# Performance work log

Measured on AMD Instinct MI355X. Metric: run time of the kernel, lower is better.

## Reference

```python
import jax, jax.numpy as jnp
import numpy as np
from jax import lax

N, IC, OC, K, SDIM, H, W = 16, 512, 512, 3, 512, 32, 32
PAD, STRIDE, LR = 1, 1, 1.0
WEIGHT_SCALER = 1.0 / np.sqrt(IC * K * K) * LR   # equalized-lr conv scale
FC_SCALER = 1.0 / np.sqrt(SDIM) * LR             # equalized-lr fc scale


def setup_inputs() -> dict:
    key = jax.random.key(0)
    k1, k2, k3 = jax.random.split(key, 3)
    x = jax.random.normal(k1, (N, IC, H, W), dtype=jnp.float32)
    style = jax.random.normal(k2, (N, SDIM), dtype=jnp.float32)
    weight = jax.random.normal(k3, (OC, IC, K, K), dtype=jnp.float32)  # std = 1/lr = 1
    fc_weight = jax.random.normal(jax.random.fold_in(key, 10), (IC, SDIM), dtype=jnp.float32)
    fc_bias = jnp.zeros((IC,), dtype=jnp.float32)
    return {"x": x, "style": style, "weight": weight,
            "fc_weight": fc_weight, "fc_bias": fc_bias}


def reference(x, style, weight, fc_weight, fc_bias):
    # EqualizedFullyConnect + AddChannelwiseBias, then +1 -> modulation rates [N, iC]
    mod = jnp.einsum('ns,cs->nc', style, fc_weight) * FC_SCALER + fc_bias * LR + 1.0
    # modulated per-sample weight [N, oC, iC, kH, kW]
    w = WEIGHT_SCALER * weight[None] * mod[:, None, :, None, None]
    # demodulate: rsqrt of sum of squares over (iC, kH, kW)
    demod = lax.rsqrt(jnp.sum(w * w, axis=(2, 3, 4)) + 1e-8)  # [N, oC]
    w = w * demod[:, :, None, None, None]
    # grouped conv with groups=N == per-sample conv: vmap over batch
    def conv1(xi, wi):
        # xi: [iC,H,W], wi: [oC,iC,kH,kW]
        return lax.conv_general_dilated(
            xi[None], wi, window_strides=(STRIDE, STRIDE),
            padding=((PAD, PAD), (PAD, PAD)),
            dimension_numbers=('NCHW', 'OIHW', 'NCHW'))[0]
    out = jax.vmap(conv1)(x, w)  # [N, oC, H, W]
    return out
```

## Files before the change

### kernel.cpp

```cpp
#include <hip/hip_runtime.h>
#include <hip/hip_bf16.h>

#define N_    16
#define IC_   512
#define OC_   512
#define SDIM_ 512
#define H_    32
#define W_    32
#define HW_   1024

#define FC_SCALER 0.04419417382415922f
#define WS_       0.014731391274719738f
#define WS2_      (1.0f/4608.0f)

typedef __attribute__((__ext_vector_type__(8)))  __bf16 bf16x8;
typedef __attribute__((__ext_vector_type__(16))) float  f32x16;
typedef __attribute__((__ext_vector_type__(4)))  int    i32x4;

typedef __attribute__((address_space(1))) const unsigned int GInt;
typedef __attribute__((address_space(3))) unsigned int LInt;

#define WAIT4()  asm volatile("s_waitcnt vmcnt(4)"  ::: "memory")
#define WAIT14() asm volatile("s_waitcnt vmcnt(14)" ::: "memory")
#define WAIT0()  asm volatile("s_waitcnt vmcnt(0)"  ::: "memory")

__device__ __forceinline__ unsigned short f2bf(float f) {
    unsigned int u = __builtin_bit_cast(unsigned int, f);
    unsigned int r = (u + 0x7FFFu + ((u >> 16) & 1u)) >> 16;
    return (unsigned short)r;
}

__global__ void k_mod(const float* __restrict__ style, const float* __restrict__ fcw,
                      const float* __restrict__ fcb, float* __restrict__ mod) {
    int gid = blockIdx.x * blockDim.x + threadIdx.x;
    int wid = gid >> 6, lane = gid & 63;
    if (wid >= N_ * IC_) return;
    int n = wid >> 9, c = wid & 511;
    const float4* sp = (const float4*)(style + n * SDIM_);
    const float4* wp = (const float4*)(fcw + (size_t)c * SDIM_);
    float acc = 0.f;
    for (int i = lane; i < SDIM_ / 4; i += 64) {
        float4 a = sp[i], b = wp[i];
        acc += a.x*b.x + a.y*b.y + a.z*b.z + a.w*b.w;
    }
#pragma unroll
    for (int off = 32; off; off >>= 1) acc += __shfl_xor(acc, off);
    if (lane == 0) mod[wid] = acc * FC_SCALER + fcb[c] + 1.0f;
}

__global__ void k_wprep(const float* __restrict__ w, unsigned short* __restrict__ wt,
                        float* __restrict__ wsq) {
    int tid = blockIdx.x * blockDim.x + threadIdx.x;
    int oc = tid >> 9, ic = tid & 511;
    int og = oc >> 7, ocl = oc & 127;
    int icc = ic >> 6, k6 = ic & 63, ks = k6 >> 3, i8 = k6 & 7;
    float s = 0.f;
#pragma unroll
    for (int t = 0; t < 9; t++) {
        float v = w[(size_t)tid * 9 + t];
        s += v * v;
        size_t off = ((((size_t)t * 4 + og) * 8 + icc) * 8192)
                   + (size_t)ks * 1024 + ocl * 8 + i8;
        wt[off] = f2bf(v);
    }
    wsq[tid] = s;
}

__global__ void k_demod(const float* __restrict__ mod, const float* __restrict__ wsq,
                        float* __restrict__ demod_ws) {
    int gid = blockIdx.x * blockDim.x + threadIdx.x;
    int wid = gid >> 6, lane = gid & 63;
    if (wid >= N_ * OC_) return;
    int n = wid >> 9, oc = wid & 511;
    const float4* mp = (const float4*)(mod + n * IC_);
    const float4* qp = (const float4*)(wsq + (size_t)oc * IC_);
    float acc = 0.f;
    for (int i = lane; i < IC_ / 4; i += 64) {
        float4 m = mp[i], q = qp[i];
        acc += m.x*m.x*q.x + m.y*m.y*q.y + m.z*m.z*q.z + m.w*m.w*q.w;
    }
#pragma unroll
    for (int off = 32; off; off >>= 1) acc += __shfl_xor(acc, off);
    if (lane == 0) {
        float s = WS2_ * acc + 1e-8f;
        demod_ws[wid] = WS_ / sqrtf(s);
    }
}

__global__ void k_premod(const float* __restrict__ x, const float* __restrict__ mod,
                         unsigned short* __restrict__ xm) {
    __shared__ __align__(16) unsigned short t_lds[64][80];
    int bx = blockIdx.x;
    int n = bx >> 7, hwt = (bx >> 3) & 15, ict = bx & 7;
    int hw0 = hwt * 64, ic0 = ict * 64;
    int tid = threadIdx.x, lane = tid & 63, ty = tid >> 6;
#pragma unroll
    for (int jj = 0; jj < 16; jj++) {
        int icl = ty * 16 + jj;
        float v = x[(size_t)(n * IC_ + ic0 + icl) * HW_ + hw0 + lane]
                  * mod[n * IC_ + ic0 + icl];
        t_lds[lane][icl] = f2bf(v);
    }
    __syncthreads();
    int xcol = tid & 31, ks = tid >> 5;
#pragma unroll
    for (int rep = 0; rep < 2; rep++) {
        int hwl = rep * 32 + xcol;
        i32x4 v = *(const i32x4*)&t_lds[hwl][ks * 8];
        int y = (hw0 >> 5) + rep;
        size_t off = ((((size_t)n * 8 + ict) * 32 + y) * 8 + ks) * 256 + xcol * 8;
        *(i32x4*)(xm + off) = v;
    }
}

__global__ __launch_bounds__(256, 1)
void k_conv(const unsigned short* __restrict__ xm, const unsigned short* __restrict__ wt,
            const float* __restrict__ demod_ws, float* __restrict__ out) {
    __shared__ __align__(16) unsigned short xt[2][10 * 2048];
    __shared__ __align__(16) unsigned short wb[3][8192];
    __shared__ __align__(16) unsigned short trash[512];
    __shared__ __align__(16) float zslot[4];
    __shared__ float s_demod[128];

    int bx = blockIdx.x;
    int octg = bx >> 6, n = (bx >> 2) & 15, spt = bx & 3;
    int oc0 = octg * 128, y0 = spt * 8;
    int tid = threadIdx.x, lane = tid & 63, wid = tid >> 6;
    int l31 = lane & 31, lhi = lane >> 5;
    int wr = wid >> 1, wc = wid & 1;

    if (tid < 128) s_demod[tid] = demod_ws[n * OC_ + oc0 + tid];
    __builtin_amdgcn_sched_barrier(0);

    if (tid == 0) { i32x4 z = {}; *(i32x4*)zslot = z; }
    if (spt == 0) {
        i32x4 z = {};
        *(i32x4*)&xt[0][tid * 8] = z;
        *(i32x4*)&xt[1][tid * 8] = z;
    }
    if (spt == 3) {
        i32x4 z = {};
        *(i32x4*)&xt[0][9 * 2048 + tid * 8] = z;
        *(i32x4*)&xt[1][9 * 2048 + tid * 8] = z;
    }

    const unsigned short* xsrc_n = xm + (size_t)n * (8 * 32 * 2048);

    auto stage_x = [&](int buf, int icc) {
        for (int wl = wid; wl < 40; wl += 4) {
            int rr = wl >> 2, q = wl & 3;
            int y = y0 - 1 + rr;
            int yc = y < 0 ? 0 : (y > 31 ? 31 : y);
            bool oob = (unsigned)y >= 32u;
            const unsigned short* g =
                xsrc_n + ((size_t)icc * 32 + yc) * 2048 + q * 512 + lane * 8;
            unsigned short* l = oob ? (unsigned short*)trash
                                    : &xt[buf][rr * 2048 + q * 512];
            __builtin_amdgcn_global_load_lds((GInt*)g, (LInt*)l, 16, 0, 0);
        }
    };
    auto stage_w = [&](int slot, int tap, int icc) {
        const unsigned short* wsrcc = wt + (((size_t)tap * 4 + octg) * 8 + icc) * 8192;
#pragma unroll
        for (int k = 0; k < 4; k++) {
            int wl = wid + k * 4;
            const unsigned short* g = wsrcc + wl * 512 + lane * 8;
            unsigned short* l = &wb[slot][wl * 512];
            __builtin_amdgcn_global_load_lds((GInt*)g, (LInt*)l, 16, 0, 0);
        }
    };

    f32x16 acc[2][4] = {};

    stage_x(0, 0);
    stage_w(0, 0, 0);
    stage_w(1, 1, 0);
    asm volatile("s_waitcnt lgkmcnt(0)" ::: "memory");

    int xb = 0;
#pragma unroll 1
    for (int icc = 0; icc < 8; icc++) {
#pragma unroll
        for (int t = 0; t < 9; t++) {
            if (t == 1 || t == 2) { if (icc < 7) WAIT14(); else WAIT4(); }
            else if (icc == 7 && t == 8) WAIT0();
            else WAIT4();
            __builtin_amdgcn_s_barrier();
            {
                int tt = t + 2;
                int wicc = icc + (tt >= 9);
                int wtap = tt >= 9 ? tt - 9 : tt;
                if (wicc < 8) stage_w((t + 2) % 3, wtap, wicc);
            }
            if (t == 0 && icc < 7) stage_x(xb ^ 1, icc + 1);

            const int dy = t / 3, dx = t % 3;
            const unsigned short* wbp = wb[t % 3];
            const unsigned short* xtp = xt[xb];
            int colbase = l31 + dx - 1;
            bool oobc = (unsigned)colbase >= 32u;
#pragma unroll
            for (int kk = 0; kk < 4; kk++) {
                int ks = kk * 2 + lhi;
                bf16x8 af[2], bfr[4];
#pragma unroll
                for (int fo = 0; fo < 2; fo++)
                    af[fo] = *(const bf16x8*)(wbp + ks * 1024 + (wr * 64 + fo * 32 + l31) * 8);
#pragma unroll
                for (int fs = 0; fs < 4; fs++) {
                    int rr = wc * 4 + fs + dy;
                    const unsigned short* p = oobc
                        ? (const unsigned short*)zslot
                        : (xtp + rr * 2048 + ks * 256 + colbase * 8);
                    bfr[fs] = *(const bf16x8*)p;
                }
                __builtin_amdgcn_s_setprio(1);
#pragma unroll
                for (int fo = 0; fo < 2; fo++)
#pragma unroll
                    for (int fs = 0; fs < 4; fs++)
                        acc[fo][fs] = __builtin_amdgcn_mfma_f32_32x32x16_bf16(
                            af[fo], bfr[fs], acc[fo][fs], 0, 0, 0);
                __builtin_amdgcn_s_setprio(0);
            }
        }
        xb ^= 1;
    }

#pragma unroll
    for (int fo = 0; fo < 2; fo++) {
#pragma unroll
        for (int fs = 0; fs < 4; fs++) {
            int y = y0 + wc * 4 + fs;
#pragma unroll
            for (int r = 0; r < 16; r++) {
                int row = (r & 3) + 8 * (r >> 2) + 4 * lhi;
                int ocl = wr * 64 + fo * 32 + row;
                float v = acc[fo][fs][r] * s_demod[ocl];
                out[((size_t)(n * OC_ + oc0 + ocl) * H_ + y) * W_ + l31] = v;
            }
        }
    }
}

extern "C" void kernel_launch(void* const* d_in, const int* in_sizes, int n_in,
                              void* d_out, int out_size, void* d_ws, size_t ws_size,
                              hipStream_t stream) {
    const float* x      = (const float*)d_in[0];
    const float* style  = (const float*)d_in[1];
    const float* weight = (const float*)d_in[2];
    const float* fcw    = (const float*)d_in[3];
    const float* fcb    = (const float*)d_in[4];
    float* out = (float*)d_out;

    char* ws = (char*)d_ws;
    float*          mod   = (float*)ws;
    float*          demod = (float*)(ws + 32768);
    float*          wsq   = (float*)(ws + 65536);
    unsigned short* wtb   = (unsigned short*)(ws + 65536 + 1048576);
    unsigned short* xmb   = (unsigned short*)(ws + 65536 + 1048576 + 4718592);

    k_mod   <<<2048, 256, 0, stream>>>(style, fcw, fcb, mod);
    k_wprep <<<1024, 256, 0, stream>>>(weight, wtb, wsq);
    k_demod <<<2048, 256, 0, stream>>>(mod, wsq, demod);
    k_premod<<<2048, 256, 0, stream>>>(x, mod, xmb);
    k_conv  <<<256,  256, 0, stream>>>(xmb, wtb, demod, out);
}
```

Before: 105.7 us.

## Split K across two wave groups and restage conv per tap column

The conv kernel goes from 256 to 512 threads. The two halves of the block each take half of every 64-channel K slice (intra-block split-K), and their partial accumulators are reduced through LDS at the end. The weight and activation layouts are re-tiled into 32-channel chunks. Each stage now loads three taps of one column and reuses six activation rows across dy, with a simpler double-buffered wait scheme. Block indices are also remapped so neighbouring blocks share n and spatial tile. The aim is more waves to hide latency and fewer LDS reads per MFMA, at the cost of a reduction epilogue and more barriers.

```diff
diff --git a/kernel.cpp b/kernel.cpp
--- a/kernel.cpp
+++ b/kernel.cpp
@@ -20,9 +20,8 @@
 typedef __attribute__((address_space(1))) const unsigned int GInt;
 typedef __attribute__((address_space(3))) unsigned int LInt;
 
-#define WAIT4()  asm volatile("s_waitcnt vmcnt(4)"  ::: "memory")
-#define WAIT14() asm volatile("s_waitcnt vmcnt(14)" ::: "memory")
 #define WAIT0()  asm volatile("s_waitcnt vmcnt(0)"  ::: "memory")
+#define WAIT3()  asm volatile("s_waitcnt vmcnt(3)"  ::: "memory")
 
 __device__ __forceinline__ unsigned short f2bf(float f) {
     unsigned int u = __builtin_bit_cast(unsigned int, f);
@@ -53,14 +52,14 @@
     int tid = blockIdx.x * blockDim.x + threadIdx.x;
     int oc = tid >> 9, ic = tid & 511;
     int og = oc >> 7, ocl = oc & 127;
-    int icc = ic >> 6, k6 = ic & 63, ks = k6 >> 3, i8 = k6 & 7;
+    int icc = ic >> 5, ks = (ic >> 3) & 3, i8 = ic & 7;
     float s = 0.f;
 #pragma unroll
     for (int t = 0; t < 9; t++) {
         float v = w[(size_t)tid * 9 + t];
         s += v * v;
-        size_t off = ((((size_t)t * 4 + og) * 8 + icc) * 8192)
-                   + (size_t)ks * 1024 + ocl * 8 + i8;
+        size_t off = ((((size_t)t * 4 + og) * 16 + icc) * 4 + ks) * 1024
+                   + (size_t)ocl * 8 + i8;
         wt[off] = f2bf(v);
     }
     wsq[tid] = s;
@@ -102,70 +101,79 @@
         t_lds[lane][icl] = f2bf(v);
     }
     __syncthreads();
-    int xcol = tid & 31, ks = tid >> 5;
+    int xcol = tid & 31, ks64 = tid >> 5;
+    int icc = ict * 2 + (ks64 >> 2), ks = ks64 & 3;
 #pragma unroll
     for (int rep = 0; rep < 2; rep++) {
         int hwl = rep * 32 + xcol;
-        i32x4 v = *(const i32x4*)&t_lds[hwl][ks * 8];
+        i32x4 v = *(const i32x4*)&t_lds[hwl][ks64 * 8];
         int y = (hw0 >> 5) + rep;
-        size_t off = ((((size_t)n * 8 + ict) * 32 + y) * 8 + ks) * 256 + xcol * 8;
+        size_t off = ((((size_t)n * 16 + icc) * 32 + y) * 4 + ks) * 256 + xcol * 8;
         *(i32x4*)(xm + off) = v;
     }
 }
 
-__global__ __launch_bounds__(256, 1)
+__global__ __launch_bounds__(512, 2)
 void k_conv(const unsigned short* __restrict__ xm, const unsigned short* __restrict__ wt,
             const float* __restrict__ demod_ws, float* __restrict__ out) {
-    __shared__ __align__(16) unsigned short xt[2][10 * 2048];
-    __shared__ __align__(16) unsigned short wb[3][8192];
-    __shared__ __align__(16) unsigned short trash[512];
-    __shared__ __align__(16) float zslot[4];
-    __shared__ float s_demod[128];
+    __shared__ __align__(16) char smem[40960 + 49152 + 1024 + 32 + 512];
+    unsigned short* xt0   = (unsigned short*)(smem);
+    unsigned short* wb0   = (unsigned short*)(smem + 40960);
+    unsigned short* trash = (unsigned short*)(smem + 90112);
+    float*          zslot = (float*)(smem + 91136);
+    float*          s_demod = (float*)(smem + 91168);
 
     int bx = blockIdx.x;
-    int octg = bx >> 6, n = (bx >> 2) & 15, spt = bx & 3;
+    int x8 = bx & 7;
+    int octg = x8 >> 1;
+    int r    = ((bx >> 3) << 1) | (x8 & 1);
+    int n = r >> 2, spt = r & 3;
     int oc0 = octg * 128, y0 = spt * 8;
+
     int tid = threadIdx.x, lane = tid & 63, wid = tid >> 6;
     int l31 = lane & 31, lhi = lane >> 5;
-    int wr = wid >> 1, wc = wid & 1;
+    int wr = wid & 1, wc = (wid >> 1) & 1, kh = wid >> 2;
 
     if (tid < 128) s_demod[tid] = demod_ws[n * OC_ + oc0 + tid];
     __builtin_amdgcn_sched_barrier(0);
 
     if (tid == 0) { i32x4 z = {}; *(i32x4*)zslot = z; }
-    if (spt == 0) {
+    if (spt == 0 && tid < 128) {
         i32x4 z = {};
-        *(i32x4*)&xt[0][tid * 8] = z;
-        *(i32x4*)&xt[1][tid * 8] = z;
-    }
-    if (spt == 3) {
+        *(i32x4*)&xt0[tid * 8] = z;
+        *(i32x4*)&xt0[10240 + tid * 8] = z;
+    }
+    if (spt == 3 && tid < 128) {
         i32x4 z = {};
-        *(i32x4*)&xt[0][9 * 2048 + tid * 8] = z;
-        *(i32x4*)&xt[1][9 * 2048 + tid * 8] = z;
-    }
-
-    const unsigned short* xsrc_n = xm + (size_t)n * (8 * 32 * 2048);
+        *(i32x4*)&xt0[9 * 1024 + tid * 8] = z;
+        *(i32x4*)&xt0[10240 + 9 * 1024 + tid * 8] = z;
+    }
+
+    const unsigned short* xsrc_n = xm + (size_t)n * (16 * 32 * 1024);
 
     auto stage_x = [&](int buf, int icc) {
-        for (int wl = wid; wl < 40; wl += 4) {
-            int rr = wl >> 2, q = wl & 3;
+#pragma unroll
+        for (int k = 0; k < 3; k++) {
+            int c = wid + k * 8;
+            int rr = c >> 1, hh = c & 1;
             int y = y0 - 1 + rr;
+            bool oob = (c >= 20) | ((unsigned)y >= 32u) | (icc >= 16);
             int yc = y < 0 ? 0 : (y > 31 ? 31 : y);
-            bool oob = (unsigned)y >= 32u;
+            int iccc = icc & 15;
             const unsigned short* g =
-                xsrc_n + ((size_t)icc * 32 + yc) * 2048 + q * 512 + lane * 8;
-            unsigned short* l = oob ? (unsigned short*)trash
-                                    : &xt[buf][rr * 2048 + q * 512];
+                xsrc_n + ((size_t)iccc * 32 + yc) * 1024 + hh * 512 + lane * 8;
+            unsigned short* l = oob ? trash
+                                    : xt0 + buf * 10240 + rr * 1024 + hh * 512;
             __builtin_amdgcn_global_load_lds((GInt*)g, (LInt*)l, 16, 0, 0);
         }
     };
-    auto stage_w = [&](int slot, int tap, int icc) {
-        const unsigned short* wsrcc = wt + (((size_t)tap * 4 + octg) * 8 + icc) * 8192;
-#pragma unroll
-        for (int k = 0; k < 4; k++) {
-            int wl = wid + k * 4;
-            const unsigned short* g = wsrcc + wl * 512 + lane * 8;
-            unsigned short* l = &wb[slot][wl * 512];
+    auto stage_w = [&](int set, int p, int icc) {
+#pragma unroll
+        for (int k = 0; k < 3; k++) {
+            int tap = k * 3 + p;
+            const unsigned short* g =
+                wt + ((((size_t)tap * 4 + octg) * 16 + icc) * 4096) + wid * 512 + lane * 8;
+            unsigned short* l = wb0 + set * 12288 + k * 4096 + wid * 512;
             __builtin_amdgcn_global_load_lds((GInt*)g, (LInt*)l, 16, 0, 0);
         }
     };
@@ -174,72 +182,81 @@
 
     stage_x(0, 0);
     stage_w(0, 0, 0);
-    stage_w(1, 1, 0);
     asm volatile("s_waitcnt lgkmcnt(0)" ::: "memory");
 
     int xb = 0;
+    int kso = kh * 2 + lhi;
 #pragma unroll 1
-    for (int icc = 0; icc < 8; icc++) {
-#pragma unroll
-        for (int t = 0; t < 9; t++) {
-            if (t == 1 || t == 2) { if (icc < 7) WAIT14(); else WAIT4(); }
-            else if (icc == 7 && t == 8) WAIT0();
-            else WAIT4();
+    for (int icc = 0; icc < 16; icc++) {
+#pragma unroll 1
+        for (int p = 0; p < 3; p++) {
+            if (p == 1) WAIT3(); else WAIT0();
             __builtin_amdgcn_s_barrier();
-            {
-                int tt = t + 2;
-                int wicc = icc + (tt >= 9);
-                int wtap = tt >= 9 ? tt - 9 : tt;
-                if (wicc < 8) stage_w((t + 2) % 3, wtap, wicc);
+            int g1 = icc * 3 + p + 1;
+            if (g1 < 48) stage_w(g1 & 1, g1 % 3, g1 / 3);
+            if (p == 0) stage_x(xb ^ 1, icc + 1);
+
+            const unsigned short* xtb = xt0 + xb * 10240;
+            const unsigned short* wbp = wb0 + ((icc * 3 + p) & 1) * 12288;
+            int col = l31 + p - 1;
+            bool oobc = (unsigned)col >= 32u;
+            bf16x8 r6[6];
+#pragma unroll
+            for (int j = 0; j < 6; j++) {
+                int rr = wc * 4 + j;
+                const unsigned short* src = oobc ? (const unsigned short*)zslot
+                    : xtb + rr * 1024 + kso * 256 + col * 8;
+                r6[j] = *(const bf16x8*)src;
             }
-            if (t == 0 && icc < 7) stage_x(xb ^ 1, icc + 1);
-
-            const int dy = t / 3, dx = t % 3;
-            const unsigned short* wbp = wb[t % 3];
-            const unsigned short* xtp = xt[xb];
-            int colbase = l31 + dx - 1;
-            bool oobc = (unsigned)colbase >= 32u;
-#pragma unroll
-            for (int kk = 0; kk < 4; kk++) {
-                int ks = kk * 2 + lhi;
-                bf16x8 af[2], bfr[4];
-#pragma unroll
-                for (int fo = 0; fo < 2; fo++)
-                    af[fo] = *(const bf16x8*)(wbp + ks * 1024 + (wr * 64 + fo * 32 + l31) * 8);
-#pragma unroll
-                for (int fs = 0; fs < 4; fs++) {
-                    int rr = wc * 4 + fs + dy;
-                    const unsigned short* p = oobc
-                        ? (const unsigned short*)zslot
-                        : (xtp + rr * 2048 + ks * 256 + colbase * 8);
-                    bfr[fs] = *(const bf16x8*)p;
-                }
+#pragma unroll
+            for (int dy = 0; dy < 3; dy++) {
+                bf16x8 af0 = *(const bf16x8*)(wbp + dy * 4096 + kso * 1024
+                                              + (wr * 64 + l31) * 8);
+                bf16x8 af1 = *(const bf16x8*)(wbp + dy * 4096 + kso * 1024
+                                              + (wr * 64 + 32 + l31) * 8);
                 __builtin_amdgcn_s_setprio(1);
 #pragma unroll
-                for (int fo = 0; fo < 2; fo++)
-#pragma unroll
-                    for (int fs = 0; fs < 4; fs++)
-                        acc[fo][fs] = __builtin_amdgcn_mfma_f32_32x32x16_bf16(
-                            af[fo], bfr[fs], acc[fo][fs], 0, 0, 0);
+                for (int fs = 0; fs < 4; fs++)
+                    acc[0][fs] = __builtin_amdgcn_mfma_f32_32x32x16_bf16(
+                        af0, r6[fs + dy], acc[0][fs], 0, 0, 0);
+#pragma unroll
+                for (int fs = 0; fs < 4; fs++)
+                    acc[1][fs] = __builtin_amdgcn_mfma_f32_32x32x16_bf16(
+                        af1, r6[fs + dy], acc[1][fs], 0, 0, 0);
                 __builtin_amdgcn_s_setprio(0);
             }
         }
         xb ^= 1;
     }
 
+    __syncthreads();
+    float* exch = (float*)smem;
 #pragma unroll
     for (int fo = 0; fo < 2; fo++) {
-#pragma unroll
-        for (int fs = 0; fs < 4; fs++) {
-            int y = y0 + wc * 4 + fs;
-#pragma unroll
-            for (int r = 0; r < 16; r++) {
-                int row = (r & 3) + 8 * (r >> 2) + 4 * lhi;
-                int ocl = wr * 64 + fo * 32 + row;
-                float v = acc[fo][fs][r] * s_demod[ocl];
-                out[((size_t)(n * OC_ + oc0 + ocl) * H_ + y) * W_ + l31] = v;
+        if (kh) {
+#pragma unroll
+            for (int fs = 0; fs < 4; fs++)
+#pragma unroll
+                for (int rg = 0; rg < 16; rg++)
+                    exch[(((wid & 3) * 4 + fs) * 16 + rg) * 64 + lane] = acc[fo][fs][rg];
+        }
+        __syncthreads();
+        if (!kh) {
+#pragma unroll
+            for (int fs = 0; fs < 4; fs++) {
+                int y = y0 + wc * 4 + fs;
+#pragma unroll
+                for (int rg = 0; rg < 16; rg++) {
+                    int row = (rg & 3) + 8 * (rg >> 2) + 4 * lhi;
+                    int ocl = wr * 64 + fo * 32 + row;
+                    float v = acc[fo][fs][rg]
+                            + exch[((wid * 4 + fs) * 16 + rg) * 64 + lane];
+                    v *= s_demod[ocl];
+                    out[((size_t)(n * OC_ + oc0 + ocl) * H_ + y) * W_ + l31] = v;
+                }
             }
         }
+        __syncthreads();
     }
 }
 
@@ -264,5 +281,5 @@
     k_wprep <<<1024, 256, 0, stream>>>(weight, wtb, wsq);
     k_demod <<<2048, 256, 0, stream>>>(mod, wsq, demod);
     k_premod<<<2048, 256, 0, stream>>>(x, mod, xmb);
-    k_conv  <<<256,  256, 0, stream>>>(xmb, wtb, demod, out);
-}
+    k_conv  <<<256,  512, 0, stream>>>(xmb, wtb, demod, out);
+}
```

Result: faster. 98.50 us (-6.8%).
